# Performance work log

Hardware: AMD Instinct MI355X
Metric: run time of the kernel (lower is better)

## Reference

```python
import jax, jax.numpy as jnp
import numpy as np


def setup_inputs() -> dict:
    key = jax.random.key(0)
    k1, k2 = jax.random.split(key)
    B, H, W, D = 16, 128, 256, 64
    UNITS = 64
    x = jax.random.normal(k1, (B, H, W, D), dtype=jnp.float32)
    w = jax.random.normal(k2, (UNITS, D), dtype=jnp.float32) * 0.05  # random_normal init
    return {"x": x, "w": w}


def reference(x, w):
    # Squared Euclidean distance from every input vector to every prototype:
    # out[b,h,w,u] = sum_d (w[u,d] - x[b,h,w,d])^2
    x2 = jnp.sum(x * x, axis=-1, keepdims=True)          # [B,H,W,1]
    w2 = jnp.sum(w * w, axis=-1)                          # [U]
    xw = jnp.einsum('bhwd,ud->bhwu', x, w)               # [B,H,W,U]
    return x2 - 2.0 * xw + w2
```

## Files before the change

kernel.cpp:

```cpp
#include <hip/hip_runtime.h>


typedef float  float4v  __attribute__((ext_vector_type(4)));
typedef __bf16 bf16x8   __attribute__((ext_vector_type(8)));

static constexpr int kRows  = 16 * 128 * 256;
static constexpr int kTiles = kRows / 16;

__device__ __forceinline__ bf16x8 cvt2(float4v a, float4v b) {
  bf16x8 r;
  r[0] = (__bf16)a[0]; r[1] = (__bf16)a[1]; r[2] = (__bf16)a[2]; r[3] = (__bf16)a[3];
  r[4] = (__bf16)b[0]; r[5] = (__bf16)b[1]; r[6] = (__bf16)b[2]; r[7] = (__bf16)b[3];
  return r;
}

__global__ __launch_bounds__(256) void sqdist_kernel(
    const float* __restrict__ X, const float* __restrict__ W,
    float* __restrict__ Out) {
  const int lane = threadIdx.x & 63;
  const int q    = lane >> 4;
  const int m    = lane & 15;

  bf16x8 aw[4][2];
  float  w2adj[4][4];
#pragma unroll
  for (int ut = 0; ut < 4; ++ut) {
    const float4v* wr = (const float4v*)(W + (ut * 16 + m) * 64);
    float4v v0 = wr[q * 2];
    float4v v1 = wr[q * 2 + 1];
    float4v v2 = wr[8 + q * 2];
    float4v v3 = wr[8 + q * 2 + 1];
    aw[ut][0] = cvt2(v0, v1);
    aw[ut][1] = cvt2(v2, v3);
    float s = 0.f;
#pragma unroll
    for (int i = 0; i < 4; ++i)
      s += v0[i] * v0[i] + v1[i] * v1[i] + v2[i] * v2[i] + v3[i] * v3[i];
    s += __shfl_xor(s, 16);
    s += __shfl_xor(s, 32);
#pragma unroll
    for (int r = 0; r < 4; ++r)
      w2adj[ut][r] = __shfl(s, q * 4 + r);
  }

  const int gw = blockIdx.x * (blockDim.x >> 6) + (threadIdx.x >> 6);
  const int nw = gridDim.x * (blockDim.x >> 6);

  for (int tile = gw; tile < kTiles; tile += nw) {
    const float4v* xr = (const float4v*)(X + (tile * 16 + m) * 64);
    float4v x0 = xr[q * 2];
    float4v x1 = xr[q * 2 + 1];
    float4v x2 = xr[8 + q * 2];
    float4v x3 = xr[8 + q * 2 + 1];

    float s = 0.f;
#pragma unroll
    for (int i = 0; i < 4; ++i)
      s += x0[i] * x0[i] + x1[i] * x1[i] + x2[i] * x2[i] + x3[i] * x3[i];
    s += __shfl_xor(s, 16);
    s += __shfl_xor(s, 32);

    bf16x8 bx0 = cvt2(x0, x1);
    bf16x8 bx1 = cvt2(x2, x3);

    float4v acc[4];
#pragma unroll
    for (int ut = 0; ut < 4; ++ut) {
      float4v z = {0.f, 0.f, 0.f, 0.f};
      acc[ut] = __builtin_amdgcn_mfma_f32_16x16x32_bf16(aw[ut][0], bx0, z, 0, 0, 0);
      acc[ut] = __builtin_amdgcn_mfma_f32_16x16x32_bf16(aw[ut][1], bx1, acc[ut], 0, 0, 0);
    }

    float4v* orow = (float4v*)(Out + (tile * 16 + m) * 64);
#pragma unroll
    for (int ut = 0; ut < 4; ++ut) {
      float4v o;
#pragma unroll
      for (int r = 0; r < 4; ++r)
        o[r] = fmaf(-2.f, acc[ut][r], s + w2adj[ut][r]);
      orow[ut * 4 + q] = o;
    }
  }
}

extern "C" void kernel_launch(void* const* d_in, const int* in_sizes, int n_in,
                              void* d_out, int out_size, void* d_ws, size_t ws_size,
                              hipStream_t stream) {
  const float* X = (const float*)d_in[0];
  const float* W = (const float*)d_in[1];
  float* Out = (float*)d_out;
  sqdist_kernel<<<1024, 256, 0, stream>>>(X, W, Out);
}
```

Before: 236.5 us.

## Prefetch X tiles into LDS with async global_load_lds multi-slot pipeline

Replaces direct per-lane global loads of X with asynchronous global_load_lds transfers into a 4-slot per-wave LDS ring buffer, using manual vmcnt waits to keep several tiles in flight. The LDS layout uses an XOR swizzle so lanes read their fragments without bank conflicts. The aim is to hide HBM latency in this memory-bound kernel through deeper prefetch. The loop is fully unrolled with a fixed iteration count tied to the grid size, and the hand-written waitcnt counts must match the number of loads outstanding.

```diff
diff --git a/kernel.cpp b/kernel.cpp
--- a/kernel.cpp
+++ b/kernel.cpp
@@ -6,6 +6,12 @@
 
 static constexpr int kRows  = 16 * 128 * 256;
 static constexpr int kTiles = kRows / 16;
+static constexpr int kWaves = 1024 * 4;
+static constexpr int kIters = kTiles / kWaves;
+static constexpr int kSlots = 4;
+
+typedef const __attribute__((address_space(1))) void gas_t;
+typedef __attribute__((address_space(3))) void las_t;
 
 __device__ __forceinline__ bf16x8 cvt2(float4v a, float4v b) {
   bf16x8 r;
@@ -17,7 +23,10 @@
 __global__ __launch_bounds__(256) void sqdist_kernel(
     const float* __restrict__ X, const float* __restrict__ W,
     float* __restrict__ Out) {
+  __shared__ float4v lds[4][kSlots][256];
+
   const int lane = threadIdx.x & 63;
+  const int wid  = threadIdx.x >> 6;
   const int q    = lane >> 4;
   const int m    = lane & 15;
 
@@ -43,15 +52,41 @@
       w2adj[ut][r] = __shfl(s, q * 4 + r);
   }
 
-  const int gw = blockIdx.x * (blockDim.x >> 6) + (threadIdx.x >> 6);
-  const int nw = gridDim.x * (blockDim.x >> 6);
+  const int gw = blockIdx.x * 4 + wid;
 
-  for (int tile = gw; tile < kTiles; tile += nw) {
-    const float4v* xr = (const float4v*)(X + (tile * 16 + m) * 64);
-    float4v x0 = xr[q * 2];
-    float4v x1 = xr[q * 2 + 1];
-    float4v x2 = xr[8 + q * 2];
-    float4v x3 = xr[8 + q * 2 + 1];
+  int soff[4];
+#pragma unroll
+  for (int c = 0; c < 4; ++c) {
+    const int r = c * 4 + q;
+    soff[c] = r * 64 + ((m ^ (r & 7)) << 2);
+  }
+
+#pragma unroll
+  for (int p = 0; p < kSlots; ++p) {
+    const float* src = X + (size_t)(gw + p * kWaves) * 1024;
+#pragma unroll
+    for (int c = 0; c < 4; ++c) {
+      __builtin_amdgcn_global_load_lds((gas_t*)(src + soff[c]),
+                                       (las_t*)&lds[wid][p][c * 64], 16, 0, 0);
+    }
+  }
+
+  const int gA = (2 * q)     ^ (m & 7);
+  const int gB = (2 * q + 1) ^ (m & 7);
+
+#pragma unroll
+  for (int k = 0; k < kIters; ++k) {
+    if (k <= 4)      asm volatile("s_waitcnt vmcnt(12)" ::: "memory");
+    else if (k == 5) asm volatile("s_waitcnt vmcnt(8)"  ::: "memory");
+    else if (k == 6) asm volatile("s_waitcnt vmcnt(4)"  ::: "memory");
+    else             asm volatile("s_waitcnt vmcnt(0)"  ::: "memory");
+    __builtin_amdgcn_sched_barrier(0);
+
+    const float4v* slot = lds[wid][k & (kSlots - 1)];
+    const float4v x0 = slot[m * 16 + gA];
+    const float4v x1 = slot[m * 16 + gB];
+    const float4v x2 = slot[m * 16 + 8 + gA];
+    const float4v x3 = slot[m * 16 + 8 + gB];
 
     float s = 0.f;
 #pragma unroll
@@ -63,6 +98,19 @@
     bf16x8 bx0 = cvt2(x0, x1);
     bf16x8 bx1 = cvt2(x2, x3);
 
+    asm volatile("s_waitcnt lgkmcnt(0)" ::: "memory");
+    __builtin_amdgcn_sched_barrier(0);
+
+    if (k + kSlots < kIters) {
+      const float* src = X + (size_t)(gw + (k + kSlots) * kWaves) * 1024;
+#pragma unroll
+      for (int c = 0; c < 4; ++c) {
+        __builtin_amdgcn_global_load_lds(
+            (gas_t*)(src + soff[c]),
+            (las_t*)&lds[wid][k & (kSlots - 1)][c * 64], 16, 0, 0);
+      }
+    }
+
     float4v acc[4];
 #pragma unroll
     for (int ut = 0; ut < 4; ++ut) {
@@ -71,7 +119,8 @@
       acc[ut] = __builtin_amdgcn_mfma_f32_16x16x32_bf16(aw[ut][1], bx1, acc[ut], 0, 0, 0);
     }
 
-    float4v* orow = (float4v*)(Out + (tile * 16 + m) * 64);
+    const int tile = gw + k * kWaves;
+    float4v* orow = (float4v*)(Out + (size_t)(tile * 16 + m) * 64);
 #pragma unroll
     for (int ut = 0; ut < 4; ++ut) {
       float4v o;
```

Measured after the change: 237.4 us. About the same (+0.4%).

## Fully unroll tile loop with triple-buffered inline-asm prefetch of X rows

Applied to the files above, without the earlier changes.

Replaces the grid-stride loop with a fixed eight-iteration unrolled schedule. Each wave keeps three register buffers of X loads in flight, issued via inline-asm global_load_dwordx4, and paces them with explicit s_waitcnt vmcnt counters. The goal is to hide global-load latency behind the MFMA and output-store work in this bandwidth-bound kernel. In exchange, the tile count and grid size are hard-coded, register pressure rises, and correctness depends on the hand-written vmcnt counts, which also count the interleaved stores.

```diff
diff --git a/kernel.cpp b/kernel.cpp
--- a/kernel.cpp
+++ b/kernel.cpp
@@ -6,6 +6,8 @@
 
 static constexpr int kRows  = 16 * 128 * 256;
 static constexpr int kTiles = kRows / 16;
+static constexpr int kWaves = 1024 * 4;
+static constexpr int kIters = kTiles / kWaves;
 
 __device__ __forceinline__ bf16x8 cvt2(float4v a, float4v b) {
   bf16x8 r;
@@ -14,10 +16,26 @@
   return r;
 }
 
+#define ISSUE(s0v, s1v, s2v, s3v, t)                                          \
+  do {                                                                        \
+    const float* p_ = X + (size_t)((t) * 16 + m) * 64 + q * 8;                \
+    asm volatile("global_load_dwordx4 %0, %4, off\n\t"                        \
+                 "global_load_dwordx4 %1, %5, off\n\t"                        \
+                 "global_load_dwordx4 %2, %6, off\n\t"                        \
+                 "global_load_dwordx4 %3, %7, off"                            \
+                 : "=&v"(s0v), "=&v"(s1v), "=&v"(s2v), "=&v"(s3v)             \
+                 : "v"(p_), "v"(p_ + 4), "v"(p_ + 32), "v"(p_ + 36));         \
+  } while (0)
+
+#define WAITC(Nstr, s0v, s1v, s2v, s3v)                                       \
+  asm volatile("s_waitcnt vmcnt(" Nstr ")"                                    \
+               : "+v"(s0v), "+v"(s1v), "+v"(s2v), "+v"(s3v)::"memory")
+
 __global__ __launch_bounds__(256) void sqdist_kernel(
     const float* __restrict__ X, const float* __restrict__ W,
     float* __restrict__ Out) {
   const int lane = threadIdx.x & 63;
+  const int wid  = threadIdx.x >> 6;
   const int q    = lane >> 4;
   const int m    = lane & 15;
 
@@ -43,16 +61,9 @@
       w2adj[ut][r] = __shfl(s, q * 4 + r);
   }
 
-  const int gw = blockIdx.x * (blockDim.x >> 6) + (threadIdx.x >> 6);
-  const int nw = gridDim.x * (blockDim.x >> 6);
+  const int gw = blockIdx.x * 4 + wid;
 
-  for (int tile = gw; tile < kTiles; tile += nw) {
-    const float4v* xr = (const float4v*)(X + (tile * 16 + m) * 64);
-    float4v x0 = xr[q * 2];
-    float4v x1 = xr[q * 2 + 1];
-    float4v x2 = xr[8 + q * 2];
-    float4v x3 = xr[8 + q * 2 + 1];
-
+  auto consume = [&](float4v x0, float4v x1, float4v x2, float4v x3, int t) {
     float s = 0.f;
 #pragma unroll
     for (int i = 0; i < 4; ++i)
@@ -71,7 +82,7 @@
       acc[ut] = __builtin_amdgcn_mfma_f32_16x16x32_bf16(aw[ut][1], bx1, acc[ut], 0, 0, 0);
     }
 
-    float4v* orow = (float4v*)(Out + (tile * 16 + m) * 64);
+    float4v* orow = (float4v*)(Out + (size_t)(t * 16 + m) * 64);
 #pragma unroll
     for (int ut = 0; ut < 4; ++ut) {
       float4v o;
@@ -80,7 +91,34 @@
         o[r] = fmaf(-2.f, acc[ut][r], s + w2adj[ut][r]);
       orow[ut * 4 + q] = o;
     }
-  }
+  };
+
+  float4v A0, A1, A2, A3, B0, B1, B2, B3, C0, C1, C2, C3;
+
+  ISSUE(A0, A1, A2, A3, gw + 0 * kWaves);
+  ISSUE(B0, B1, B2, B3, gw + 1 * kWaves);
+  ISSUE(C0, C1, C2, C3, gw + 2 * kWaves);
+
+  WAITC("8", A0, A1, A2, A3);  consume(A0, A1, A2, A3, gw + 0 * kWaves);
+  ISSUE(A0, A1, A2, A3, gw + 3 * kWaves);
+
+  WAITC("8", B0, B1, B2, B3);  consume(B0, B1, B2, B3, gw + 1 * kWaves);
+  ISSUE(B0, B1, B2, B3, gw + 4 * kWaves);
+
+  WAITC("8", C0, C1, C2, C3);  consume(C0, C1, C2, C3, gw + 2 * kWaves);
+  ISSUE(C0, C1, C2, C3, gw + 5 * kWaves);
+
+  WAITC("8", A0, A1, A2, A3);  consume(A0, A1, A2, A3, gw + 3 * kWaves);
+  ISSUE(A0, A1, A2, A3, gw + 6 * kWaves);
+
+  WAITC("8", B0, B1, B2, B3);  consume(B0, B1, B2, B3, gw + 4 * kWaves);
+  ISSUE(B0, B1, B2, B3, gw + 7 * kWaves);
+
+  WAITC("8", C0, C1, C2, C3);  consume(C0, C1, C2, C3, gw + 5 * kWaves);
+
+  WAITC("4", A0, A1, A2, A3);  consume(A0, A1, A2, A3, gw + 6 * kWaves);
+
+  WAITC("0", B0, B1, B2, B3);  consume(B0, B1, B2, B3, gw + 7 * kWaves);
 }
 
 extern "C" void kernel_launch(void* const* d_in, const int* in_sizes, int n_in,
```

New measurement: 234.8 us. About the same (-0.7%).
